# Performance work log

Measured on AMD Instinct MI355X. Metric: run time of the kernel, lower is better.

## Reference

```python
import jax, jax.numpy as jnp
import numpy as np

NH = 16          # num_attention_heads
NOPE = 128       # qk_nope_head_dim
ROPE = 64        # qk_rope_head_dim
QHD = NOPE + ROPE  # q_head_dim = 192
VD = 128         # v_head_dim
QLR = 1536       # q_lora_rank
KVLR = 512       # kv_lora_rank
HID = 2048
B, S = 1, 2048
THETA = 10000.0
EPS = 1e-6


def rms_norm(x, w, eps=EPS):
    xf = x.astype(jnp.float32)
    var = jnp.mean(xf * xf, axis=-1, keepdims=True)
    return (w * (xf * jax.lax.rsqrt(var + eps)).astype(x.dtype))


def _deinterleave(x):
    # view(..., d//2, 2).transpose(-1, -2).reshape(..., d): evens then odds
    return jnp.concatenate([x[..., 0::2], x[..., 1::2]], axis=-1)


def _rotate_half(x):
    h = x.shape[-1] // 2
    return jnp.concatenate([-x[..., h:], x[..., :h]], axis=-1)


def setup_inputs() -> dict:
    key = jax.random.key(0)
    ks = jax.random.split(key, 6)
    s = 0.02
    return {
        'hidden_states': jax.random.normal(ks[0], (B, S, HID), jnp.float32),
        'position_ids': jnp.arange(S, dtype=jnp.int32)[None, :],
        'Wqa': jax.random.normal(ks[1], (HID, QLR), jnp.float32) * s,
        'qa_ln_w': jnp.ones((QLR,), jnp.float32),
        'Wqb': jax.random.normal(ks[2], (QLR, NH * QHD), jnp.float32) * s,
        'Wkva': jax.random.normal(ks[3], (HID, KVLR + ROPE), jnp.float32) * s,
        'kv_ln_w': jnp.ones((KVLR,), jnp.float32),
        'Wkvb': jax.random.normal(ks[4], (KVLR, NH * (NOPE + VD)), jnp.float32) * s,
        'Wo': jax.random.normal(ks[5], (NH * VD, HID), jnp.float32) * s,
    }


def reference(hidden_states, position_ids, Wqa, qa_ln_w, Wqb, Wkva, kv_ln_w, Wkvb, Wo):
    b, s, _ = hidden_states.shape
    # Q path: low-rank down -> RMSNorm -> up
    q = rms_norm(hidden_states @ Wqa, qa_ln_w) @ Wqb
    q = q.reshape(b, s, NH, QHD).transpose(0, 2, 1, 3)          # (b,h,s,192)
    q_nope, q_pe = q[..., :NOPE], q[..., NOPE:]
    # KV path: compressed kv + shared rope key
    ckv = hidden_states @ Wkva                                   # (b,s,576)
    c_kv, k_pe = ckv[..., :KVLR], ckv[..., KVLR:]
    k_pe = k_pe.reshape(b, s, 1, ROPE).transpose(0, 2, 1, 3)     # (b,1,s,64)
    kv = rms_norm(c_kv, kv_ln_w) @ Wkvb
    kv = kv.reshape(b, s, NH, NOPE + VD).transpose(0, 2, 1, 3)   # (b,h,s,256)
    k_nope, v = kv[..., :NOPE], kv[..., NOPE:]
    # partial RoPE on the 64-dim rope slices
    inv_freq = 1.0 / (THETA ** (jnp.arange(0, ROPE, 2, dtype=jnp.float32) / ROPE))
    t = jnp.arange(s, dtype=jnp.float32)
    emb = jnp.concatenate([jnp.outer(t, inv_freq)] * 2, axis=-1)  # (s,64)
    cos = jnp.cos(emb)[position_ids][:, None]                     # (b,1,s,64)
    sin = jnp.sin(emb)[position_ids][:, None]
    q_pe = _deinterleave(q_pe)
    k_pe = _deinterleave(k_pe)
    q_pe = q_pe * cos + _rotate_half(q_pe) * sin
    k_pe = k_pe * cos + _rotate_half(k_pe) * sin
    query = jnp.concatenate([q_nope, q_pe], axis=-1)                       # (b,h,s,192)
    key = jnp.concatenate([k_nope, jnp.broadcast_to(k_pe, (b, NH, s, ROPE))], axis=-1)
    # causal attention, softmax_scale = q_head_dim**-0.5
    scale = QHD ** (-0.5)
    scores = jnp.einsum('bhqd,bhkd->bhqk', query, key) * scale
    mask = jnp.tril(jnp.ones((s, s), dtype=bool))
    scores = jnp.where(mask, scores, jnp.finfo(scores.dtype).min)
    probs = jax.nn.softmax(scores, axis=-1)
    attn = jnp.einsum('bhqk,bhkd->bhqd', probs, v)               # (b,h,s,128)
    out = attn.transpose(0, 2, 1, 3).reshape(b, s, NH * VD) @ Wo  # (b,s,hid)
    return out
```

## Files before the change

### kernel.cpp

```cpp
#include <hip/hip_runtime.h>
#include <hip/hip_bf16.h>

typedef unsigned short u16;
typedef _Float16 h16;
typedef h16 h16x8 __attribute__((ext_vector_type(8)));
typedef h16 h16x4 __attribute__((ext_vector_type(4)));
typedef float f32x4 __attribute__((ext_vector_type(4)));

#define S_LEN 2048
#define QLR   1536
#define KVLR  512
#define NHEAD 16
#define QHD   192
#define QHS   200
#define VDIM  128
#define SCALE 0.07216878364870322f
#define FREQC (-0.4152410118609203f)

__device__ __forceinline__ void gld16(const h16* g, h16* l){
  __builtin_amdgcn_global_load_lds((__attribute__((address_space(1))) const void*)g,
                                   (__attribute__((address_space(3))) void*)l, 16, 0, 0);
}

__global__ __launch_bounds__(256) void k_prep(const float* __restrict__ hidden, h16* __restrict__ hb,
      const float* __restrict__ Wqa, const float* __restrict__ Wkva, const float* __restrict__ Wqb,
      const float* __restrict__ Wkvb, const float* __restrict__ Wo,
      h16* __restrict__ Wc, h16* __restrict__ WqbT, h16* __restrict__ WkvbT, h16* __restrict__ WoT){
  int bx = blockIdx.x;
  const int tid = threadIdx.x;
  if (bx < 4096){
    int i = bx*256 + tid;
    float4 v = ((const float4*)hidden)[i];
    h16x4 o = { (h16)v.x, (h16)v.y, (h16)v.z, (h16)v.w };
    ((h16x4*)hb)[i] = o;
    return;
  }
  bx -= 4096;
  const float* W; h16* WT; int K, N, nx;
  if (bx < 768)       { W = Wqa;  WT = Wc;                K = 2048; N = 1536; nx = 24; }
  else if (bx < 1056) { bx -= 768;  W = Wkva; WT = Wc + 1536ull*2048; K = 2048; N = 576;  nx = 9;  }
  else if (bx < 2208) { bx -= 1056; W = Wqb;  WT = WqbT;  K = 1536; N = 3072; nx = 48; }
  else if (bx < 2720) { bx -= 2208; W = Wkvb; WT = WkvbT; K = 512;  N = 4096; nx = 64; }
  else                { bx -= 2720; W = Wo;   WT = WoT;   K = 2048; N = 2048; nx = 32; }
  int ty = bx / nx, tx = bx - ty*nx;
  int k0 = ty * 64, n0 = tx * 64;
  __shared__ float t[64][65];
  int r = tid >> 4, c4 = (tid & 15) * 4;
#pragma unroll
  for (int it = 0; it < 4; it++){
    float4 v = *(const float4*)(W + (size_t)(k0 + it*16 + r) * N + n0 + c4);
    t[it*16+r][c4] = v.x; t[it*16+r][c4+1] = v.y; t[it*16+r][c4+2] = v.z; t[it*16+r][c4+3] = v.w;
  }
  __syncthreads();
  int n = tid >> 2, k16 = (tid & 3) * 16;
  h16x8 o0, o1;
#pragma unroll
  for (int e = 0; e < 8; e++){ o0[e] = (h16)t[k16 + e][n]; o1[e] = (h16)t[k16 + 8 + e][n]; }
  h16* dst = WT + (size_t)(n0 + n) * K + k0 + k16;
  *(h16x8*)dst = o0;
  *(h16x8*)(dst + 8) = o1;
}

__device__ __forceinline__ void gemm_core(const h16* __restrict__ A, const h16* __restrict__ B,
    int K, int m0, int n0, h16* As, h16* Bs, f32x4 (&acc)[4][4]){
  const int tid = threadIdx.x;
  const int lane = tid & 63, quad = lane >> 4, lr = lane & 15;
  const int wid = tid >> 6;
  const int wr = (wid >> 1) * 64, wc = (wid & 1) * 64;
  const int sr = tid >> 2, scc = (tid & 3) * 8;
  const h16* Ag = A + (size_t)(m0 + sr) * K + scc;
  const h16* Bg = B + (size_t)(n0 + sr) * K + scc;
  for (int kt = 0; kt < K; kt += 32){
    gld16(Ag + kt,                 &As[tid * 8]);
    gld16(Ag + (size_t)64*K + kt,  &As[2048 + tid * 8]);
    gld16(Bg + kt,                 &Bs[tid * 8]);
    gld16(Bg + (size_t)64*K + kt,  &Bs[2048 + tid * 8]);
    __syncthreads();
    h16x8 af[4], bfr[4];
#pragma unroll
    for (int r = 0; r < 4; r++) af[r]  = *(const h16x8*)&As[(wr + r*16 + lr) * 32 + quad * 8];
#pragma unroll
    for (int c = 0; c < 4; c++) bfr[c] = *(const h16x8*)&Bs[(wc + c*16 + lr) * 32 + quad * 8];
#pragma unroll
    for (int r = 0; r < 4; r++)
#pragma unroll
      for (int c = 0; c < 4; c++)
        acc[r][c] = __builtin_amdgcn_mfma_f32_16x16x32_f16(af[r], bfr[c], acc[r][c], 0, 0, 0);
    __syncthreads();
  }
}

template<bool OF32>
__global__ __launch_bounds__(256) void k_gemm(const h16* __restrict__ A, const h16* __restrict__ B,
                                              void* __restrict__ Cv, int N, int K){
  __shared__ __attribute__((aligned(16))) h16 As[128*32];
  __shared__ __attribute__((aligned(16))) h16 Bs[128*32];
  const int m0 = blockIdx.y * 128, n0 = blockIdx.x * 128;
  f32x4 acc[4][4] = {};
  gemm_core(A, B, K, m0, n0, As, Bs, acc);
  const int lane = threadIdx.x & 63, quad = lane >> 4, lr = lane & 15;
  const int wid = threadIdx.x >> 6;
  const int wr = (wid >> 1) * 64, wc = (wid & 1) * 64;
#pragma unroll
  for (int r = 0; r < 4; r++)
#pragma unroll
    for (int c = 0; c < 4; c++){
      int row = m0 + wr + r*16 + quad*4;
      int col = n0 + wc + c*16 + lr;
#pragma unroll
      for (int i = 0; i < 4; i++){
        float val = acc[r][c][i];
        if (OF32) ((float*)Cv)[(size_t)(row + i) * N + col] = val;
        else      ((h16*)Cv)[(size_t)(row + i) * N + col] = (h16)val;
      }
    }
}

__global__ __launch_bounds__(256) void k_gemm_qkv(const h16* __restrict__ qln, const h16* __restrict__ WqbT,
      const h16* __restrict__ kvln, const h16* __restrict__ WkvbT,
      h16* __restrict__ Qh, h16* __restrict__ Kh, h16* __restrict__ VT,
      const float* __restrict__ cst, const float* __restrict__ snt){
  __shared__ __attribute__((aligned(16))) h16 As[128*32];
  __shared__ __attribute__((aligned(16))) h16 Bs[128*32];
  __shared__ __attribute__((aligned(16))) h16 tsm[128*132];
  const int m0 = blockIdx.y * 128;
  const int tid = threadIdx.x;
  const int lane = tid & 63, quad = lane >> 4, lr = lane & 15;
  const int wid = tid >> 6;
  const int wr = (wid >> 1) * 64, wc = (wid & 1) * 64;
  f32x4 acc[4][4] = {};
  if (blockIdx.x < 24){
    const int n0 = blockIdx.x * 128;
    gemm_core(qln, WqbT, QLR, m0, n0, As, Bs, acc);
#pragma unroll
    for (int r = 0; r < 4; r++)
#pragma unroll
      for (int c = 0; c < 4; c++){
        int row0 = m0 + wr + r*16 + quad*4;
        int cg = n0 + wc + c*16 + lr;
        int head = cg / 192;
        int inner = cg - head*192;
        h16* outb = Qh + ((size_t)head*S_LEN)*QHS;
        if (inner < 128){
#pragma unroll
          for (int i = 0; i < 4; i++)
            outb[(size_t)(row0+i)*QHS + inner] = (h16)(acc[r][c][i] * SCALE);
        } else {
          int d = (inner - 128) >> 1;
          int isY = inner & 1;
          int ocol = (isY ? 160 : 128) + d;
#pragma unroll
          for (int i = 0; i < 4; i++){
            int rr = row0 + i;
            float cs = cst[rr*32 + d], sn = snt[rr*32 + d];
            float v = acc[r][c][i];
            float w = __shfl_xor(v, 1);
            float out = isY ? (v*cs + w*sn) : (v*cs - w*sn);
            outb[(size_t)rr*QHS + ocol] = (h16)(out * SCALE);
          }
        }
      }
  } else {
    const int n0 = (blockIdx.x - 24) * 128;
    gemm_core(kvln, WkvbT, KVLR, m0, n0, As, Bs, acc);
    const int head = n0 >> 8;
    if ((n0 & 128) == 0){
#pragma unroll
      for (int r = 0; r < 4; r++)
#pragma unroll
        for (int c = 0; c < 4; c++){
          int row0 = m0 + wr + r*16 + quad*4;
          int inner = wc + c*16 + lr;
#pragma unroll
          for (int i = 0; i < 4; i++)
            Kh[((size_t)head*S_LEN + row0 + i)*QHS + inner] = (h16)acc[r][c][i];
        }
    } else {
#pragma unroll
      for (int r = 0; r < 4; r++)
#pragma unroll
        for (int c = 0; c < 4; c++){
          int lrow = wr + r*16 + quad*4;
          int dv = wc + c*16 + lr;
#pragma unroll
          for (int i = 0; i < 4; i++)
            tsm[(lrow + i)*132 + dv] = (h16)acc[r][c][i];
        }
      __syncthreads();
      int dv = tid >> 1, sh = (tid & 1) * 64;
      h16* vout = VT + ((size_t)(head*VDIM + dv))*S_LEN + m0 + sh;
#pragma unroll
      for (int ko = 0; ko < 8; ko++){
        h16x8 o;
#pragma unroll
        for (int e = 0; e < 8; e++) o[e] = tsm[(sh + ko*8 + e)*132 + dv];
        *(h16x8*)(vout + ((ko*8 + 8*(dv & 7)) & 63)) = o;
      }
    }
  }
}

__global__ __launch_bounds__(256) void k_norm(const h16* __restrict__ Cc,
      const float* __restrict__ qw, const float* __restrict__ kw, const int* __restrict__ pos_ids,
      h16* __restrict__ qln, h16* __restrict__ kvln, h16* __restrict__ Kh,
      float* __restrict__ cst, float* __restrict__ snt){
  const int s = blockIdx.x, tid = threadIdx.x;
  __shared__ float red[8];
  __shared__ h16 kpe_s[64];
  const h16* c1 = Cc + (size_t)s * 2176;
  float v[6]; float ss = 0.f;
#pragma unroll
  for (int i = 0; i < 6; i++){ v[i] = (float)c1[tid + i*256]; ss += v[i]*v[i]; }
  for (int off = 32; off > 0; off >>= 1) ss += __shfl_down(ss, off);
  if ((tid & 63) == 0) red[tid >> 6] = ss;
  __syncthreads();
  float rq = rsqrtf((red[0]+red[1]+red[2]+red[3]) / (float)QLR + 1e-6f);
#pragma unroll
  for (int i = 0; i < 6; i++)
    qln[(size_t)s * QLR + tid + i*256] = (h16)(qw[tid + i*256] * v[i] * rq);

  const h16* ck = c1 + QLR;
  float w0 = (float)ck[tid], w1 = (float)ck[tid + 256];
  float ss2 = w0*w0 + w1*w1;
  for (int off = 32; off > 0; off >>= 1) ss2 += __shfl_down(ss2, off);
  if ((tid & 63) == 0) red[4 + (tid >> 6)] = ss2;
  __syncthreads();
  float rk = rsqrtf((red[4]+red[5]+red[6]+red[7]) / (float)KVLR + 1e-6f);
  kvln[(size_t)s * KVLR + tid]       = (h16)(kw[tid] * w0 * rk);
  kvln[(size_t)s * KVLR + tid + 256] = (h16)(kw[tid + 256] * w1 * rk);

  if (tid < 32){
    int d = tid;
    float x = (float)ck[KVLR + 2*d];
    float y = (float)ck[KVLR + 2*d + 1];
    float a = (float)pos_ids[s] * exp2f(FREQC * (float)d);
    float cs = cosf(a), sn = sinf(a);
    cst[s*32 + d] = cs; snt[s*32 + d] = sn;
    kpe_s[d]      = (h16)(x*cs - y*sn);
    kpe_s[32 + d] = (h16)(y*cs + x*sn);
  }
  __syncthreads();
  {
    int h = tid >> 4, seg = (tid & 15) * 4;
    h16x4 o = { kpe_s[seg], kpe_s[seg+1], kpe_s[seg+2], kpe_s[seg+3] };
    *(h16x4*)&Kh[((size_t)h*S_LEN + s)*QHS + 128 + seg] = o;
  }
}

__global__ __launch_bounds__(256, 2) void k_flash(const h16* __restrict__ Qh, const h16* __restrict__ Kh,
      const h16* __restrict__ VT, h16* __restrict__ Opart, float* __restrict__ ml){
  const int tile = 15 - blockIdx.x;
  const int h = blockIdx.y;
  const int p = blockIdx.z;
  const int jcount = 2*tile + 2;
  const int jlo = p * 8;
  if (jlo >= jcount) return;
  const int jhi = min(jlo + 8, jcount);
  const int m0 = tile * 128;
  __shared__ __attribute__((aligned(16))) h16 Ksm[64*QHS];
  __shared__ __attribute__((aligned(16))) h16 Vsm[144*64];
  __shared__ __attribute__((aligned(16))) h16 Psm[128*72];
  const int tid = threadIdx.x, wid = tid >> 6, lane = tid & 63, quad = lane >> 4, lr = lane & 15;

  {
    h16x4 one4 = { (h16)1.f, (h16)1.f, (h16)1.f, (h16)1.f };
    *(h16x4*)&Vsm[128*64 + tid*4] = one4;
  }

  const h16* Qbase = Qh + ((size_t)h*S_LEN + m0)*QHS;
  h16x8 qf[2][6];
#pragma unroll
  for (int rt = 0; rt < 2; rt++)
#pragma unroll
    for (int ks = 0; ks < 6; ks++)
      qf[rt][ks] = *(const h16x8*)(Qbase + (size_t)(wid*32 + rt*16 + lr)*QHS + ks*32 + quad*8);

  float mst[2][4];
  f32x4 oacc[2][9] = {};
#pragma unroll
  for (int rt = 0; rt < 2; rt++)
#pragma unroll
    for (int i = 0; i < 4; i++) mst[rt][i] = -1e30f;

  for (int j = jlo; j < jhi; ++j){
    const h16* Kg = Kh + ((size_t)h*S_LEN + j*64)*QHS;
#pragma unroll
    for (int i = 0; i < 6; i++) gld16(Kg + i*2048 + tid*8, &Ksm[i*2048 + tid*8]);
    if (tid < 64) gld16(Kg + 12288 + tid*8, &Ksm[12288 + tid*8]);
    const h16* Vg = VT + (size_t)h * VDIM * S_LEN + (size_t)j * 64;
#pragma unroll
    for (int i = 0; i < 4; i++)
      gld16(Vg + (size_t)(i*32 + (tid >> 3)) * S_LEN + (tid & 7)*8, &Vsm[i*2048 + tid*8]);
    __syncthreads();

    f32x4 sc[2][4] = {};
#pragma unroll
    for (int ks = 0; ks < 6; ks++)
#pragma unroll
      for (int ct = 0; ct < 4; ct++){
        h16x8 kf = *(const h16x8*)&Ksm[(ct*16 + lr)*QHS + ks*32 + quad*8];
        sc[0][ct] = __builtin_amdgcn_mfma_f32_16x16x32_f16(qf[0][ks], kf, sc[0][ct], 0,0,0);
        sc[1][ct] = __builtin_amdgcn_mfma_f32_16x16x32_f16(qf[1][ks], kf, sc[1][ct], 0,0,0);
      }

    if (j >= 2*tile){
#pragma unroll
      for (int rt = 0; rt < 2; rt++)
#pragma unroll
        for (int ct = 0; ct < 4; ct++){
          int kcol = j*64 + ct*16 + lr;
#pragma unroll
          for (int i = 0; i < 4; i++)
            if (kcol > m0 + wid*32 + rt*16 + quad*4 + i) sc[rt][ct][i] = -1e30f;
        }
    }

#pragma unroll
    for (int rt = 0; rt < 2; rt++){
      float al[4];
#pragma unroll
      for (int i = 0; i < 4; i++){
        float m = fmaxf(fmaxf(sc[rt][0][i], sc[rt][1][i]), fmaxf(sc[rt][2][i], sc[rt][3][i]));
#pragma unroll
        for (int off = 1; off < 16; off <<= 1) m = fmaxf(m, __shfl_xor(m, off));
        float mn = fmaxf(fmaxf(mst[rt][i], m), -1e29f);
        al[i] = __expf(mst[rt][i] - mn);
        mst[rt][i] = mn;
      }
#pragma unroll
      for (int ct = 0; ct < 4; ct++)
#pragma unroll
        for (int i = 0; i < 4; i++)
          Psm[(wid*32 + rt*16 + quad*4 + i)*72 + ct*16 + lr] = (h16)__expf(sc[rt][ct][i] - mst[rt][i]);
#pragma unroll
      for (int oc = 0; oc < 9; oc++)
#pragma unroll
        for (int i = 0; i < 4; i++) oacc[rt][oc][i] *= al[i];
    }

#pragma unroll
    for (int ks2 = 0; ks2 < 2; ks2++){
      h16x8 pf0 = *(const h16x8*)&Psm[(wid*32 + lr)*72      + ks2*32 + quad*8];
      h16x8 pf1 = *(const h16x8*)&Psm[(wid*32 + 16 + lr)*72 + ks2*32 + quad*8];
      int cv = (ks2*32 + quad*8 + 8*(lr & 7)) & 63;
#pragma unroll
      for (int oc = 0; oc < 9; oc++){
        h16x8 vf = *(const h16x8*)&Vsm[(oc*16 + lr)*64 + cv];
        oacc[0][oc] = __builtin_amdgcn_mfma_f32_16x16x32_f16(pf0, vf, oacc[0][oc], 0,0,0);
        oacc[1][oc] = __builtin_amdgcn_mfma_f32_16x16x32_f16(pf1, vf, oacc[1][oc], 0,0,0);
      }
    }
    __syncthreads();
  }

  const int part = (tile*NHEAD + h)*4 + p;
  h16* Op = Opart + (size_t)part * 16384;
#pragma unroll
  for (int rt = 0; rt < 2; rt++){
#pragma unroll
    for (int oc = 0; oc < 8; oc++)
#pragma unroll
      for (int i = 0; i < 4; i++)
        Op[(wid*32 + rt*16 + quad*4 + i)*128 + oc*16 + lr] = (h16)oacc[rt][oc][i];
    if (lr == 0){
#pragma unroll
      for (int i = 0; i < 4; i++){
        int r = wid*32 + rt*16 + quad*4 + i;
        ml[(size_t)part*256 + r*2]     = mst[rt][i];
        ml[(size_t)part*256 + r*2 + 1] = oacc[rt][8][i];
      }
    }
  }
}

__global__ __launch_bounds__(256) void k_comb(const h16* __restrict__ Opart, const float* __restrict__ ml,
                                              h16* __restrict__ Ob){
  const int t = blockIdx.x, h = blockIdx.y, tid = threadIdx.x;
  const int P = (2*t + 9) >> 3;
  const int r = tid >> 1, c0 = (tid & 1) * 64;
  const int base = (t*NHEAD + h)*4;
  float w[4]; float M = -1e30f, denom = 0.f;
  for (int p = 0; p < P; p++) M = fmaxf(M, ml[(size_t)(base+p)*256 + r*2]);
  for (int p = 0; p < P; p++){
    w[p] = __expf(ml[(size_t)(base+p)*256 + r*2] - M);
    denom += w[p] * ml[(size_t)(base+p)*256 + r*2 + 1];
  }
  float inv = 1.f / denom;
#pragma unroll
  for (int ch = 0; ch < 8; ch++){
    float a[8] = {};
    for (int p = 0; p < P; p++){
      h16x8 v = *(const h16x8*)&Opart[(size_t)(base+p)*16384 + r*128 + c0 + ch*8];
#pragma unroll
      for (int e = 0; e < 8; e++) a[e] += w[p] * (float)v[e];
    }
    h16x8 o;
#pragma unroll
    for (int e = 0; e < 8; e++) o[e] = (h16)(a[e] * inv);
    *(h16x8*)&Ob[((size_t)(t*128 + r))*(NHEAD*VDIM) + h*VDIM + c0 + ch*8] = o;
  }
}

extern "C" void kernel_launch(void* const* d_in, const int* in_sizes, int n_in,
                              void* d_out, int out_size, void* d_ws, size_t ws_size,
                              hipStream_t stream){
  const float* hidden = (const float*)d_in[0];
  const int*   pos    = (const int*)  d_in[1];
  const float* Wqa    = (const float*)d_in[2];
  const float* qaw    = (const float*)d_in[3];
  const float* Wqb    = (const float*)d_in[4];
  const float* Wkva   = (const float*)d_in[5];
  const float* kvw    = (const float*)d_in[6];
  const float* Wkvb   = (const float*)d_in[7];
  const float* Wo     = (const float*)d_in[8];

  h16* ws = (h16*)d_ws;
  size_t off = 0;
  auto take = [&](size_t n){ h16* p = ws + off; off += n; return p; };
  h16* hb    = take(2048ull * 2048);
  h16* WoT   = take(2048ull * 2048);
  h16* Wc    = take(2176ull * 2048);
  h16* WqbT  = take(3072ull * 1536);
  h16* WkvbT = take(4096ull * 512);
  h16* Ccomb = take(2048ull * 2176);
  h16* qln   = take(2048ull * 1536);
  h16* kvln  = take(2048ull * 512);
  float* cst = (float*)take(2048ull * 64);
  float* snt = (float*)take(2048ull * 64);
  h16* Qh    = take(16ull * 2048 * QHS);
  h16* Kh    = take(16ull * 2048 * QHS);
  h16* VT    = take(16ull * 128 * 2048);
  h16* Ob    = hb;
  h16*   Opart = Wc;
  float* mlbuf = (float*)(Wc + 16ull*16*4*16384);

  k_prep<<<7840, 256, 0, stream>>>(hidden, hb, Wqa, Wkva, Wqb, Wkvb, Wo, Wc, WqbT, WkvbT, WoT);
  k_gemm<false><<<dim3(17, 16), 256, 0, stream>>>(hb, Wc, Ccomb, 2176, 2048);
  k_norm<<<2048, 256, 0, stream>>>(Ccomb, qaw, kvw, pos, qln, kvln, Kh, cst, snt);
  k_gemm_qkv<<<dim3(56, 16), 256, 0, stream>>>(qln, WqbT, kvln, WkvbT, Qh, Kh, VT, cst, snt);
  k_flash<<<dim3(16, 16, 4), 256, 0, stream>>>(Qh, Kh, VT, Opart, mlbuf);
  k_comb<<<dim3(16, 16), 256, 0, stream>>>(Opart, mlbuf, Ob);
  k_gemm<true><<<dim3(16, 16), 256, 0, stream>>>(Ob, WoT, d_out, 2048, 2048);
}
```

Measured before the change: 376.7 us.

## Use 64-row GEMM tiles, shrink flash P buffer, alias qkv LDS, raise occupancy

The down-projection and output GEMMs now use 64x128 tiles with twice as many blocks, to fill more compute units on a 2048-row problem. The flash kernel writes P in two 32-column halves, halving its P shared buffer, and asks for 3 blocks per SM instead of 2. The qkv GEMM reuses the A/B staging LDS for the V transpose buffer, storing it transposed with vector writes to cut LDS use and per-element stores. Smaller tiles lower per-block data reuse, and the tighter launch bound may cause register spills in the flash kernel.

```diff
diff --git a/kernel.cpp b/kernel.cpp
--- a/kernel.cpp
+++ b/kernel.cpp
@@ -61,28 +61,29 @@
   *(h16x8*)(dst + 8) = o1;
 }
 
-__device__ __forceinline__ void gemm_core(const h16* __restrict__ A, const h16* __restrict__ B,
-    int K, int m0, int n0, h16* As, h16* Bs, f32x4 (&acc)[4][4]){
+template<int MB>
+__device__ __forceinline__ void gemm_coreT(const h16* __restrict__ A, const h16* __restrict__ B,
+    int K, int m0, int n0, h16* As, h16* Bs, f32x4 (&acc)[MB/32][4]){
   const int tid = threadIdx.x;
   const int lane = tid & 63, quad = lane >> 4, lr = lane & 15;
   const int wid = tid >> 6;
-  const int wr = (wid >> 1) * 64, wc = (wid & 1) * 64;
+  const int wr = (wid >> 1) * (MB/2), wc = (wid & 1) * 64;
   const int sr = tid >> 2, scc = (tid & 3) * 8;
   const h16* Ag = A + (size_t)(m0 + sr) * K + scc;
   const h16* Bg = B + (size_t)(n0 + sr) * K + scc;
   for (int kt = 0; kt < K; kt += 32){
-    gld16(Ag + kt,                 &As[tid * 8]);
-    gld16(Ag + (size_t)64*K + kt,  &As[2048 + tid * 8]);
+    gld16(Ag + kt, &As[tid * 8]);
+    if (MB == 128) gld16(Ag + (size_t)64*K + kt, &As[2048 + tid * 8]);
     gld16(Bg + kt,                 &Bs[tid * 8]);
     gld16(Bg + (size_t)64*K + kt,  &Bs[2048 + tid * 8]);
     __syncthreads();
-    h16x8 af[4], bfr[4];
-#pragma unroll
-    for (int r = 0; r < 4; r++) af[r]  = *(const h16x8*)&As[(wr + r*16 + lr) * 32 + quad * 8];
+    h16x8 af[MB/32], bfr[4];
+#pragma unroll
+    for (int r = 0; r < MB/32; r++) af[r] = *(const h16x8*)&As[(wr + r*16 + lr) * 32 + quad * 8];
 #pragma unroll
     for (int c = 0; c < 4; c++) bfr[c] = *(const h16x8*)&Bs[(wc + c*16 + lr) * 32 + quad * 8];
 #pragma unroll
-    for (int r = 0; r < 4; r++)
+    for (int r = 0; r < MB/32; r++)
 #pragma unroll
       for (int c = 0; c < 4; c++)
         acc[r][c] = __builtin_amdgcn_mfma_f32_16x16x32_f16(af[r], bfr[c], acc[r][c], 0, 0, 0);
@@ -90,19 +91,19 @@
   }
 }
 
-template<bool OF32>
+template<bool OF32, int MB>
 __global__ __launch_bounds__(256) void k_gemm(const h16* __restrict__ A, const h16* __restrict__ B,
                                               void* __restrict__ Cv, int N, int K){
-  __shared__ __attribute__((aligned(16))) h16 As[128*32];
+  __shared__ __attribute__((aligned(16))) h16 As[MB*32];
   __shared__ __attribute__((aligned(16))) h16 Bs[128*32];
-  const int m0 = blockIdx.y * 128, n0 = blockIdx.x * 128;
-  f32x4 acc[4][4] = {};
-  gemm_core(A, B, K, m0, n0, As, Bs, acc);
+  const int m0 = blockIdx.y * MB, n0 = blockIdx.x * 128;
+  f32x4 acc[MB/32][4] = {};
+  gemm_coreT<MB>(A, B, K, m0, n0, As, Bs, acc);
   const int lane = threadIdx.x & 63, quad = lane >> 4, lr = lane & 15;
   const int wid = threadIdx.x >> 6;
-  const int wr = (wid >> 1) * 64, wc = (wid & 1) * 64;
-#pragma unroll
-  for (int r = 0; r < 4; r++)
+  const int wr = (wid >> 1) * (MB/2), wc = (wid & 1) * 64;
+#pragma unroll
+  for (int r = 0; r < MB/32; r++)
 #pragma unroll
     for (int c = 0; c < 4; c++){
       int row = m0 + wr + r*16 + quad*4;
@@ -120,9 +121,9 @@
       const h16* __restrict__ kvln, const h16* __restrict__ WkvbT,
       h16* __restrict__ Qh, h16* __restrict__ Kh, h16* __restrict__ VT,
       const float* __restrict__ cst, const float* __restrict__ snt){
-  __shared__ __attribute__((aligned(16))) h16 As[128*32];
-  __shared__ __attribute__((aligned(16))) h16 Bs[128*32];
-  __shared__ __attribute__((aligned(16))) h16 tsm[128*132];
+  __shared__ __attribute__((aligned(16))) h16 smem[16896];
+  h16* As = smem;
+  h16* Bs = smem + 4096;
   const int m0 = blockIdx.y * 128;
   const int tid = threadIdx.x;
   const int lane = tid & 63, quad = lane >> 4, lr = lane & 15;
@@ -131,7 +132,7 @@
   f32x4 acc[4][4] = {};
   if (blockIdx.x < 24){
     const int n0 = blockIdx.x * 128;
-    gemm_core(qln, WqbT, QLR, m0, n0, As, Bs, acc);
+    gemm_coreT<128>(qln, WqbT, QLR, m0, n0, As, Bs, acc);
 #pragma unroll
     for (int r = 0; r < 4; r++)
 #pragma unroll
@@ -162,7 +163,7 @@
       }
   } else {
     const int n0 = (blockIdx.x - 24) * 128;
-    gemm_core(kvln, WkvbT, KVLR, m0, n0, As, Bs, acc);
+    gemm_coreT<128>(kvln, WkvbT, KVLR, m0, n0, As, Bs, acc);
     const int head = n0 >> 8;
     if ((n0 & 128) == 0){
 #pragma unroll
@@ -176,25 +177,25 @@
             Kh[((size_t)head*S_LEN + row0 + i)*QHS + inner] = (h16)acc[r][c][i];
         }
     } else {
+      h16* tsm = smem;
 #pragma unroll
       for (int r = 0; r < 4; r++)
 #pragma unroll
         for (int c = 0; c < 4; c++){
-          int lrow = wr + r*16 + quad*4;
           int dv = wc + c*16 + lr;
-#pragma unroll
-          for (int i = 0; i < 4; i++)
-            tsm[(lrow + i)*132 + dv] = (h16)acc[r][c][i];
+          int row0 = wr + r*16 + quad*4;
+          h16x4 o = { (h16)acc[r][c][0], (h16)acc[r][c][1], (h16)acc[r][c][2], (h16)acc[r][c][3] };
+          *(h16x4*)&tsm[dv*132 + row0] = o;
         }
       __syncthreads();
-      int dv = tid >> 1, sh = (tid & 1) * 64;
-      h16* vout = VT + ((size_t)(head*VDIM + dv))*S_LEN + m0 + sh;
-#pragma unroll
-      for (int ko = 0; ko < 8; ko++){
-        h16x8 o;
-#pragma unroll
-        for (int e = 0; e < 8; e++) o[e] = tsm[(sh + ko*8 + e)*132 + dv];
-        *(h16x8*)(vout + ((ko*8 + 8*(dv & 7)) & 63)) = o;
+      int dv = tid >> 1, half = tid & 1;
+      h16* vout = VT + ((size_t)(head*VDIM + dv))*S_LEN + m0 + half*64;
+#pragma unroll
+      for (int k = 0; k < 8; k++){
+        h16x4 a = *(const h16x4*)&tsm[dv*132 + half*64 + k*8];
+        h16x4 b = *(const h16x4*)&tsm[dv*132 + half*64 + k*8 + 4];
+        h16x8 v = { a[0],a[1],a[2],a[3], b[0],b[1],b[2],b[3] };
+        *(h16x8*)(vout + ((k*8 + 8*(dv & 7)) & 63)) = v;
       }
     }
   }
@@ -247,7 +248,7 @@
   }
 }
 
-__global__ __launch_bounds__(256, 2) void k_flash(const h16* __restrict__ Qh, const h16* __restrict__ Kh,
+__global__ __launch_bounds__(256, 3) void k_flash(const h16* __restrict__ Qh, const h16* __restrict__ Kh,
       const h16* __restrict__ VT, h16* __restrict__ Opart, float* __restrict__ ml){
   const int tile = 15 - blockIdx.x;
   const int h = blockIdx.y;
@@ -259,7 +260,7 @@
   const int m0 = tile * 128;
   __shared__ __attribute__((aligned(16))) h16 Ksm[64*QHS];
   __shared__ __attribute__((aligned(16))) h16 Vsm[144*64];
-  __shared__ __attribute__((aligned(16))) h16 Psm[128*72];
+  __shared__ __attribute__((aligned(16))) h16 Psm[128*36];
   const int tid = threadIdx.x, wid = tid >> 6, lane = tid & 63, quad = lane >> 4, lr = lane & 15;
 
   {
@@ -328,21 +329,25 @@
         mst[rt][i] = mn;
       }
 #pragma unroll
-      for (int ct = 0; ct < 4; ct++)
-#pragma unroll
-        for (int i = 0; i < 4; i++)
-          Psm[(wid*32 + rt*16 + quad*4 + i)*72 + ct*16 + lr] = (h16)__expf(sc[rt][ct][i] - mst[rt][i]);
-#pragma unroll
       for (int oc = 0; oc < 9; oc++)
 #pragma unroll
         for (int i = 0; i < 4; i++) oacc[rt][oc][i] *= al[i];
     }
 
 #pragma unroll
-    for (int ks2 = 0; ks2 < 2; ks2++){
-      h16x8 pf0 = *(const h16x8*)&Psm[(wid*32 + lr)*72      + ks2*32 + quad*8];
-      h16x8 pf1 = *(const h16x8*)&Psm[(wid*32 + 16 + lr)*72 + ks2*32 + quad*8];
-      int cv = (ks2*32 + quad*8 + 8*(lr & 7)) & 63;
+    for (int c2 = 0; c2 < 2; c2++){
+#pragma unroll
+      for (int rt = 0; rt < 2; rt++)
+#pragma unroll
+        for (int cc = 0; cc < 2; cc++){
+          int ct = c2*2 + cc;
+#pragma unroll
+          for (int i = 0; i < 4; i++)
+            Psm[(wid*32 + rt*16 + quad*4 + i)*36 + cc*16 + lr] = (h16)__expf(sc[rt][ct][i] - mst[rt][i]);
+        }
+      h16x8 pf0 = *(const h16x8*)&Psm[(wid*32 + lr)*36      + quad*8];
+      h16x8 pf1 = *(const h16x8*)&Psm[(wid*32 + 16 + lr)*36 + quad*8];
+      int cv = (c2*32 + quad*8 + 8*(lr & 7)) & 63;
 #pragma unroll
       for (int oc = 0; oc < 9; oc++){
         h16x8 vf = *(const h16x8*)&Vsm[(oc*16 + lr)*64 + cv];
@@ -435,10 +440,10 @@
   float* mlbuf = (float*)(Wc + 16ull*16*4*16384);
 
   k_prep<<<7840, 256, 0, stream>>>(hidden, hb, Wqa, Wkva, Wqb, Wkvb, Wo, Wc, WqbT, WkvbT, WoT);
-  k_gemm<false><<<dim3(17, 16), 256, 0, stream>>>(hb, Wc, Ccomb, 2176, 2048);
+  k_gemm<false,64><<<dim3(17, 32), 256, 0, stream>>>(hb, Wc, Ccomb, 2176, 2048);
   k_norm<<<2048, 256, 0, stream>>>(Ccomb, qaw, kvw, pos, qln, kvln, Kh, cst, snt);
   k_gemm_qkv<<<dim3(56, 16), 256, 0, stream>>>(qln, WqbT, kvln, WkvbT, Qh, Kh, VT, cst, snt);
   k_flash<<<dim3(16, 16, 4), 256, 0, stream>>>(Qh, Kh, VT, Opart, mlbuf);
   k_comb<<<dim3(16, 16), 256, 0, stream>>>(Opart, mlbuf, Ob);
-  k_gemm<true><<<dim3(16, 16), 256, 0, stream>>>(Ob, WoT, d_out, 2048, 2048);
-}
+  k_gemm<true,64><<<dim3(16, 32), 256, 0, stream>>>(Ob, WoT, d_out, 2048, 2048);
+}
```

Result: slower. 406.4 us (+7.9%).
